# Kernel optimization log

Measured on AMD Instinct MI355X. Metric: run time of the kernel, lower is better.

## Reference

```python
import jax, jax.numpy as jnp
import numpy as np

N_HEAD = 12
N_EMBD = 768
N_EMBD_SIDE = 384
N_EMBD_KQ = 192
N_EMBD_OUT = N_EMBD + N_EMBD_SIDE  # 1152
B, L = 2, 2048


def setup_inputs() -> dict:
    key = jax.random.key(0)
    ks = jax.random.split(key, 12)
    s = 0.02
    return {
        "x": jax.random.normal(ks[0], (B, L, N_EMBD), dtype=jnp.float32),
        "side": jax.random.normal(ks[1], (B, L, N_EMBD_SIDE), dtype=jnp.float32),
        # weights stored as (in_features, out_features) so y = x @ W + b
        "Wq": jax.random.normal(ks[2], (N_EMBD_SIDE, N_EMBD_KQ), dtype=jnp.float32) * s,
        "bq": jnp.zeros((N_EMBD_KQ,), dtype=jnp.float32),
        "Wkv": jax.random.normal(ks[3], (N_EMBD_OUT, N_EMBD_KQ + N_EMBD_OUT), dtype=jnp.float32) * s,
        "bkv": jnp.zeros((N_EMBD_KQ + N_EMBD_OUT,), dtype=jnp.float32),
        "Wproj": jax.random.normal(ks[4], (N_EMBD_OUT, N_EMBD_OUT), dtype=jnp.float32) * s,
        "bproj": jnp.zeros((N_EMBD_OUT,), dtype=jnp.float32),
        "Wemb": jax.random.normal(ks[5], (N_EMBD_SIDE, N_EMBD_OUT), dtype=jnp.float32) * s,
        "bemb": jnp.zeros((N_EMBD_OUT,), dtype=jnp.float32),
    }


def reference(x, side, Wq, bq, Wkv, bkv, Wproj, bproj, Wemb, bemb):
    batch, length, _ = x.shape
    hd_kq = N_EMBD_KQ // N_HEAD   # 16
    hd_v = N_EMBD_OUT // N_HEAD   # 96

    q = (side @ Wq + bq).reshape(batch, length, N_HEAD, hd_kq).transpose(0, 2, 1, 3)  # [B,H,L,dk]
    kv = jnp.concatenate((x, side), axis=2) @ Wkv + bkv
    k = kv[:, :, :N_EMBD_KQ].reshape(batch, length, N_HEAD, hd_kq).transpose(0, 2, 1, 3)
    v = kv[:, :, N_EMBD_KQ:].reshape(batch, length, N_HEAD, hd_v).transpose(0, 2, 1, 3)

    first = (side[:, 0] @ Wemb + bemb).reshape(batch, N_HEAD, 1, hd_v)  # [B,H,1,dv]

    # shifted causal mask: row i attends to j < i; row 0 copies row 1 (attends to j==0)
    mask = jnp.tril(jnp.ones((length, length), dtype=bool), k=-1)
    mask = mask.at[0].set(mask[1])

    scale = 1.0 / jnp.sqrt(jnp.asarray(hd_kq, dtype=q.dtype))
    scores = jnp.einsum("bhqd,bhkd->bhqk", q, k) * scale
    scores = jnp.where(mask, scores, -jnp.inf)
    attn = jax.nn.softmax(scores, axis=-1)
    y = jnp.einsum("bhqk,bhkd->bhqd", attn, v)  # [B,H,L,dv]

    # special-case first token: replaced by learned embedding of side[:,0]
    y = jnp.concatenate((first, y[:, :, 1:]), axis=2)
    y = y.transpose(0, 2, 1, 3).reshape(batch, length, N_EMBD_OUT)
    return y @ Wproj + bproj
```

## Files before the change

### kernel.cpp

```cpp
#include <hip/hip_runtime.h>
#include <hip/hip_bf16.h>
#include <math.h>

#define N_HEADS 12
#define L_SEQ   2048
#define BATCH   2
#define D_KQ    192
#define D_OUT   1152
#define D_KV    1344
#define D_X     768
#define D_SIDE  384
#define HD_K    16
#define HD_V    96
#define M_ROWS  4096

typedef __attribute__((ext_vector_type(8))) short bf16x8;
typedef __attribute__((ext_vector_type(4))) float f32x4;

__device__ inline float  b2f(ushort u){ union{uint i; float f;} v; v.i=(uint)u<<16; return v.f; }
__device__ inline ushort f2b(float f){ __hip_bfloat16 h = __float2bfloat16(f);
                                       return *reinterpret_cast<ushort*>(&h); }

__device__ inline void gload_lds16(const ushort* g, ushort* l) {
    __builtin_amdgcn_global_load_lds(
        (const __attribute__((address_space(1))) void*)g,
        (__attribute__((address_space(3))) void*)l, 16, 0, 0);
}

#define SWZ(r, c) ((((r) * 64) + (c)) ^ (((r) & 7) << 3))

__global__ __launch_bounds__(256)
void cvt_f32_bf16(const float* __restrict__ src, int sstride,
                  ushort* __restrict__ dst, int dstride, int w4, int rows) {
    int gid = blockIdx.x * 256 + threadIdx.x;
    if (gid >= w4 * rows) return;
    int r = gid / w4, c = gid - r * w4;
    float4 v = *reinterpret_cast<const float4*>(&src[(size_t)r * sstride + c * 4]);
    ushort4 o = make_ushort4(f2b(v.x), f2b(v.y), f2b(v.z), f2b(v.w));
    *reinterpret_cast<ushort4*>(&dst[(size_t)r * dstride + c * 4]) = o;
}

__global__ __launch_bounds__(256)
void transpose_cvt(const float* __restrict__ W, ushort* __restrict__ Wt,
                   int K, int N, int Npad) {
    __shared__ float t[32][33];
    const int n0 = blockIdx.x * 32, k0 = blockIdx.y * 32;
    const int tx = threadIdx.x & 31, ty = threadIdx.x >> 5;
#pragma unroll
    for (int i = 0; i < 4; i++) {
        int n = n0 + tx;
        t[ty + i * 8][tx] = (n < N) ? W[(size_t)(k0 + ty + i * 8) * N + n] : 0.f;
    }
    __syncthreads();
#pragma unroll
    for (int i = 0; i < 4; i++) {
        int n = n0 + ty + i * 8;
        Wt[(size_t)n * K + k0 + tx] = f2b(t[tx][ty + i * 8]);
    }
}

template<int STORE_BF16>
__global__ __launch_bounds__(256)
void gemm_mfma(const ushort* __restrict__ A, const ushort* __restrict__ Bt,
               const float* __restrict__ bias, void* __restrict__ Cv,
               int M, int N, int K) {
    __shared__ ushort As[128 * 32];
    __shared__ ushort Bs[128 * 32];
    const int tid = threadIdx.x;
    const int w = tid >> 6, lane = tid & 63;
    const int wr = w >> 1, wc = w & 1;
    const int n0 = blockIdx.x * 128, m0 = blockIdx.y * 128;
    const int l4 = lane & 3, lrow = lane >> 2;
    const int kgrp = lane >> 4, l16 = lane & 15;

    f32x4 acc[4][4];
#pragma unroll
    for (int i = 0; i < 4; i++)
#pragma unroll
        for (int j = 0; j < 4; j++)
            acc[i][j] = (f32x4){0.f, 0.f, 0.f, 0.f};

    for (int kt = 0; kt < K; kt += 32) {
        __syncthreads();
#pragma unroll
        for (int r = 0; r < 2; r++) {
            const int seg = r * 4 + w;
            const int trow = seg * 16 + lrow;
            gload_lds16(&A [(size_t)(m0 + trow) * K + kt + l4 * 8], &As[seg * 512]);
            gload_lds16(&Bt[(size_t)(n0 + trow) * K + kt + l4 * 8], &Bs[seg * 512]);
        }
        __syncthreads();

        bf16x8 a[4], b[4];
#pragma unroll
        for (int i = 0; i < 4; i++)
            a[i] = *reinterpret_cast<const bf16x8*>(
                &As[(wr * 64 + i * 16 + l16) * 32 + kgrp * 8]);
#pragma unroll
        for (int j = 0; j < 4; j++)
            b[j] = *reinterpret_cast<const bf16x8*>(
                &Bs[(wc * 64 + j * 16 + l16) * 32 + kgrp * 8]);
#pragma unroll
        for (int i = 0; i < 4; i++)
#pragma unroll
            for (int j = 0; j < 4; j++)
                acc[i][j] = __builtin_amdgcn_mfma_f32_16x16x32_bf16(
                    a[i], b[j], acc[i][j], 0, 0, 0);
    }

    const int rgrp = lane >> 4;
#pragma unroll
    for (int j = 0; j < 4; j++) {
        const int col = n0 + wc * 64 + j * 16 + l16;
        if (col >= N) continue;
        const float bv = bias[col];
#pragma unroll
        for (int i = 0; i < 4; i++) {
            const int row0 = m0 + wr * 64 + i * 16 + rgrp * 4;
#pragma unroll
            for (int rg = 0; rg < 4; rg++) {
                float v = acc[i][j][rg] + bv;
                if (STORE_BF16)
                    ((ushort*)Cv)[(size_t)(row0 + rg) * N + col] = f2b(v);
                else
                    ((float*)Cv)[(size_t)(row0 + rg) * N + col] = v;
            }
        }
    }
}

__global__ __launch_bounds__(256)
void attn_mfma(const ushort* __restrict__ qb, const ushort* __restrict__ kvb,
               ushort* __restrict__ yb) {
    __shared__ ushort Ks2[64 * 40];
    __shared__ ushort Vt[96 * 64];
    __shared__ ushort Ps[4][16 * 64];

    const int tid  = threadIdx.x;
    const int w    = tid >> 6, lane = tid & 63;
    const int l16  = lane & 15, kgrp = lane >> 4;

    const int item = blockIdx.x;
    const int qt = item & 31, hb = item >> 5;
    const int h  = hb % N_HEADS, b = hb / N_HEADS;

    const ushort* kvbase = kvb + (size_t)b * L_SEQ * D_KV;
    const int rowbase = qt * 64;

    bf16x8 qf = {0, 0, 0, 0, 0, 0, 0, 0};
    if (kgrp < 2)
        qf = *reinterpret_cast<const bf16x8*>(
            qb + ((size_t)b * L_SEQ + rowbase + w * 16 + l16) * D_KQ + h * HD_K + kgrp * 8);

    float m[4] = {-INFINITY, -INFINITY, -INFINITY, -INFINITY};
    float l[4] = {0.f, 0.f, 0.f, 0.f};
    f32x4 acc[6];
#pragma unroll
    for (int ob = 0; ob < 6; ob++) acc[ob] = (f32x4){0.f, 0.f, 0.f, 0.f};

    for (int t2 = 0; t2 <= qt; t2++) {
        const int j0 = t2 * 64;
        const bool diag = (t2 == qt);
        __syncthreads();

        {
            const int key = tid >> 2, c = (tid & 3) * 4;
            ushort4 k4 = *reinterpret_cast<const ushort4*>(
                kvbase + (size_t)(j0 + key) * D_KV + h * HD_K + c);
            *reinterpret_cast<ushort4*>(&Ks2[key * 40 + c])      = k4;
            *reinterpret_cast<ushort4*>(&Ks2[key * 40 + 16 + c]) = make_ushort4(0, 0, 0, 0);
        }
        {
            const int key = tid >> 2, d0 = (tid & 3) * 24;
            const uint4* vsrc = reinterpret_cast<const uint4*>(
                kvbase + (size_t)(j0 + key) * D_KV + D_KQ + h * HD_V + d0);
#pragma unroll
            for (int ch = 0; ch < 3; ch++) {
                uint4 u = vsrc[ch];
                const int d = d0 + ch * 8;
                Vt[SWZ(d + 0, key)] = (ushort)(u.x & 0xffff);
                Vt[SWZ(d + 1, key)] = (ushort)(u.x >> 16);
                Vt[SWZ(d + 2, key)] = (ushort)(u.y & 0xffff);
                Vt[SWZ(d + 3, key)] = (ushort)(u.y >> 16);
                Vt[SWZ(d + 4, key)] = (ushort)(u.z & 0xffff);
                Vt[SWZ(d + 5, key)] = (ushort)(u.z >> 16);
                Vt[SWZ(d + 6, key)] = (ushort)(u.w & 0xffff);
                Vt[SWZ(d + 7, key)] = (ushort)(u.w >> 16);
            }
        }
        __syncthreads();

        f32x4 s[4];
#pragma unroll
        for (int f = 0; f < 4; f++) {
            bf16x8 kf = *reinterpret_cast<const bf16x8*>(
                &Ks2[(f * 16 + l16) * 40 + kgrp * 8]);
            s[f] = __builtin_amdgcn_mfma_f32_16x16x32_bf16(
                qf, kf, (f32x4){0.f, 0.f, 0.f, 0.f}, 0, 0, 0);
        }

#pragma unroll
        for (int f = 0; f < 4; f++)
#pragma unroll
            for (int r = 0; r < 4; r++) {
                float v = s[f][r] * 0.25f;
                if (diag) {
                    const int row64 = w * 16 + kgrp * 4 + r;
                    const int key64 = f * 16 + l16;
                    if (key64 >= row64) v = -INFINITY;
                }
                s[f][r] = v;
            }

        float scl[4];
#pragma unroll
        for (int r = 0; r < 4; r++) {
            float mt = fmaxf(fmaxf(s[0][r], s[1][r]), fmaxf(s[2][r], s[3][r]));
            mt = fmaxf(mt, __shfl_xor(mt, 1));
            mt = fmaxf(mt, __shfl_xor(mt, 2));
            mt = fmaxf(mt, __shfl_xor(mt, 4));
            mt = fmaxf(mt, __shfl_xor(mt, 8));
            const float mn = fmaxf(m[r], mt);
            scl[r] = __expf(m[r] - mn);
            m[r] = mn;
            float ps = 0.f;
#pragma unroll
            for (int f = 0; f < 4; f++) {
                float p = __expf(s[f][r] - mn);
                s[f][r] = p;
                ps += p;
            }
            ps += __shfl_xor(ps, 1);
            ps += __shfl_xor(ps, 2);
            ps += __shfl_xor(ps, 4);
            ps += __shfl_xor(ps, 8);
            l[r] = l[r] * scl[r] + ps;
        }

#pragma unroll
        for (int f = 0; f < 4; f++)
#pragma unroll
            for (int r = 0; r < 4; r++)
                Ps[w][SWZ(kgrp * 4 + r, f * 16 + l16)] = f2b(s[f][r]);
#pragma unroll
        for (int ob = 0; ob < 6; ob++)
#pragma unroll
            for (int r = 0; r < 4; r++)
                acc[ob][r] *= scl[r];

        asm volatile("s_waitcnt lgkmcnt(0)" ::: "memory");
        __builtin_amdgcn_sched_barrier(0);

        bf16x8 pa0 = *reinterpret_cast<const bf16x8*>(&Ps[w][SWZ(l16, kgrp * 8)]);
        bf16x8 pa1 = *reinterpret_cast<const bf16x8*>(&Ps[w][SWZ(l16, 32 + kgrp * 8)]);
#pragma unroll
        for (int ob = 0; ob < 6; ob++) {
            bf16x8 vb0 = *reinterpret_cast<const bf16x8*>(&Vt[SWZ(ob * 16 + l16, kgrp * 8)]);
            bf16x8 vb1 = *reinterpret_cast<const bf16x8*>(&Vt[SWZ(ob * 16 + l16, 32 + kgrp * 8)]);
            acc[ob] = __builtin_amdgcn_mfma_f32_16x16x32_bf16(pa0, vb0, acc[ob], 0, 0, 0);
            acc[ob] = __builtin_amdgcn_mfma_f32_16x16x32_bf16(pa1, vb1, acc[ob], 0, 0, 0);
        }
    }

#pragma unroll
    for (int r = 0; r < 4; r++) {
        const float inv = 1.f / l[r];
        ushort* dst = yb + ((size_t)b * L_SEQ + rowbase + w * 16 + kgrp * 4 + r) * D_OUT
                        + h * HD_V;
#pragma unroll
        for (int ob = 0; ob < 6; ob++)
            dst[ob * 16 + l16] = f2b(acc[ob][r] * inv);
    }
}

__global__ __launch_bounds__(128)
void first_kernel(const float* __restrict__ side, const float* __restrict__ Wemb,
                  const float* __restrict__ bemb, ushort* __restrict__ yb) {
    const int o = blockIdx.x * 128 + threadIdx.x;
    const int b = blockIdx.y;
    const float* s = side + (size_t)b * L_SEQ * D_SIDE;
    float acc = bemb[o];
    for (int k = 0; k < D_SIDE; k++)
        acc += s[k] * Wemb[(size_t)k * D_OUT + o];
    yb[(size_t)b * L_SEQ * D_OUT + o] = f2b(acc);
}

extern "C" void kernel_launch(void* const* d_in, const int* in_sizes, int n_in,
                              void* d_out, int out_size, void* d_ws, size_t ws_size,
                              hipStream_t stream) {
    const float* x     = (const float*)d_in[0];
    const float* side  = (const float*)d_in[1];
    const float* Wq    = (const float*)d_in[2];
    const float* bq    = (const float*)d_in[3];
    const float* Wkv   = (const float*)d_in[4];
    const float* bkv   = (const float*)d_in[5];
    const float* Wproj = (const float*)d_in[6];
    const float* bproj = (const float*)d_in[7];
    const float* Wemb  = (const float*)d_in[8];
    const float* bemb  = (const float*)d_in[9];
    float* out = (float*)d_out;

    char* ws = (char*)d_ws;
    ushort* xs_bf   = (ushort*)(ws + 0);
    ushort* side_bf = (ushort*)(ws + 9437184);
    ushort* wq_t    = (ushort*)(ws + 12582912);
    ushort* wkv_t   = (ushort*)(ws + 12779520);
    ushort* wproj_t = (ushort*)(ws + 16023552);
    ushort* qbuf    = (ushort*)(ws + 18677760);
    ushort* kvbuf   = (ushort*)(ws + 20250624);
    ushort* ybuf    = (ushort*)(ws + 31260672);

    {
        int items_x  = (D_X / 4) * M_ROWS;
        int items_sd = (D_SIDE / 4) * M_ROWS;
        cvt_f32_bf16<<<(items_x  + 255) / 256, 256, 0, stream>>>(
            x,    D_X,    xs_bf,       D_OUT,  D_X / 4,    M_ROWS);
        cvt_f32_bf16<<<(items_sd + 255) / 256, 256, 0, stream>>>(
            side, D_SIDE, xs_bf + D_X, D_OUT,  D_SIDE / 4, M_ROWS);
        cvt_f32_bf16<<<(items_sd + 255) / 256, 256, 0, stream>>>(
            side, D_SIDE, side_bf,     D_SIDE, D_SIDE / 4, M_ROWS);
    }
    transpose_cvt<<<dim3(8, 12),  256, 0, stream>>>(Wq,    wq_t,    D_SIDE, D_KQ,  256);
    transpose_cvt<<<dim3(44, 36), 256, 0, stream>>>(Wkv,   wkv_t,   D_OUT,  D_KV,  1408);
    transpose_cvt<<<dim3(36, 36), 256, 0, stream>>>(Wproj, wproj_t, D_OUT,  D_OUT, 1152);

    gemm_mfma<1><<<dim3(2, 32),  256, 0, stream>>>(side_bf, wq_t,    bq,    qbuf,  M_ROWS, D_KQ,  D_SIDE);
    gemm_mfma<1><<<dim3(11, 32), 256, 0, stream>>>(xs_bf,   wkv_t,   bkv,   kvbuf, M_ROWS, D_KV,  D_OUT);
    attn_mfma<<<768, 256, 0, stream>>>(qbuf, kvbuf, ybuf);
    first_kernel<<<dim3(9, BATCH), 128, 0, stream>>>(side, Wemb, bemb, ybuf);
    gemm_mfma<0><<<dim3(9, 32),  256, 0, stream>>>(ybuf,    wproj_t, bproj, out,   M_ROWS, D_OUT, D_OUT);
}
```

Before: 321.9 us.

## Emit transposed V and separate K from KV GEMM; DMA tiles into LDS

The KV projection GEMM now writes K to its own row-major buffer and V pre-transposed per (batch, head) into a swizzled-compatible layout. The attention kernel can then fill its K and V tiles with direct global-to-LDS loads instead of scalar transposing stores. The attention grid is also remapped so heavy and light causal tiles are interleaved, and MFMA sections are bracketed with s_setprio. The risk is less coalesced epilogue stores in the GEMM, which writes V with strided ushort4 stores, and correctness depends on the voff swizzle matching SWZ.

Measured after the change: 280.1 us. -13.0%, faster.

```diff
diff --git a/kernel.cpp b/kernel.cpp
--- a/kernel.cpp
+++ b/kernel.cpp
@@ -59,11 +59,11 @@
     }
 }
 
-template<int STORE_BF16>
+template<int MODE>
 __global__ __launch_bounds__(256)
 void gemm_mfma(const ushort* __restrict__ A, const ushort* __restrict__ Bt,
                const float* __restrict__ bias, void* __restrict__ Cv,
-               int M, int N, int K) {
+               ushort* __restrict__ vt, int M, int N, int K) {
     __shared__ ushort As[128 * 32];
     __shared__ ushort Bs[128 * 32];
     const int tid = threadIdx.x;
@@ -114,13 +114,40 @@
         const int col = n0 + wc * 64 + j * 16 + l16;
         if (col >= N) continue;
         const float bv = bias[col];
+        if constexpr (MODE == 2) {
+            if (col >= D_KQ) {
+                const int hh = (col - D_KQ) / HD_V;
+                const int dd = (col - D_KQ) % HD_V;
+                const int bb = m0 >> 11;
+                ushort* vrow = vt + ((size_t)(bb * N_HEADS + hh) * HD_V + dd) * L_SEQ
+                                  + (m0 & 2047);
+#pragma unroll
+                for (int i = 0; i < 4; i++) {
+                    const int r0 = wr * 64 + i * 16 + rgrp * 4;
+                    ushort4 o = make_ushort4(
+                        f2b(acc[i][j][0] + bv), f2b(acc[i][j][1] + bv),
+                        f2b(acc[i][j][2] + bv), f2b(acc[i][j][3] + bv));
+                    *reinterpret_cast<ushort4*>(&vrow[r0]) = o;
+                }
+                continue;
+            }
+#pragma unroll
+            for (int i = 0; i < 4; i++) {
+                const int row0 = m0 + wr * 64 + i * 16 + rgrp * 4;
+#pragma unroll
+                for (int rg = 0; rg < 4; rg++)
+                    ((ushort*)Cv)[(size_t)(row0 + rg) * D_KQ + col] =
+                        f2b(acc[i][j][rg] + bv);
+            }
+            continue;
+        }
 #pragma unroll
         for (int i = 0; i < 4; i++) {
             const int row0 = m0 + wr * 64 + i * 16 + rgrp * 4;
 #pragma unroll
             for (int rg = 0; rg < 4; rg++) {
                 float v = acc[i][j][rg] + bv;
-                if (STORE_BF16)
+                if (MODE == 1)
                     ((ushort*)Cv)[(size_t)(row0 + rg) * N + col] = f2b(v);
                 else
                     ((float*)Cv)[(size_t)(row0 + rg) * N + col] = v;
@@ -130,27 +157,47 @@
 }
 
 __global__ __launch_bounds__(256)
-void attn_mfma(const ushort* __restrict__ qb, const ushort* __restrict__ kvb,
-               ushort* __restrict__ yb) {
-    __shared__ ushort Ks2[64 * 40];
+void attn_mfma(const ushort* __restrict__ qbuf, const ushort* __restrict__ kb,
+               const ushort* __restrict__ vtg, ushort* __restrict__ yb) {
     __shared__ ushort Vt[96 * 64];
+    __shared__ ushort Ks[64 * 16];
+    __shared__ __align__(16) ushort Kz[8];
     __shared__ ushort Ps[4][16 * 64];
 
-    const int tid  = threadIdx.x;
-    const int w    = tid >> 6, lane = tid & 63;
-    const int l16  = lane & 15, kgrp = lane >> 4;
-
-    const int item = blockIdx.x;
-    const int qt = item & 31, hb = item >> 5;
-    const int h  = hb % N_HEADS, b = hb / N_HEADS;
-
-    const ushort* kvbase = kvb + (size_t)b * L_SEQ * D_KV;
+    const int tid = threadIdx.x;
+    const int w = tid >> 6, lane = tid & 63;
+    const int l16 = lane & 15, kgrp = lane >> 4;
+
+    const int i = blockIdx.x, jj5 = i & 255, g = i >> 8;
+    const int q5 = jj5 & 31;
+    const int qt = (g == 0) ? q5 : (g == 1) ? (31 - q5) : ((q5 + 16) & 31);
+    const int hb = g * 8 + (jj5 >> 5);
+    const int h = hb % N_HEADS, b = hb / N_HEADS;
+
+    if (tid < 8) Kz[tid] = 0;
+
+    const ushort* vt_h  = vtg + (size_t)(b * N_HEADS + h) * HD_V * L_SEQ;
+    const ushort* kbase = kb + (size_t)b * L_SEQ * D_KQ;
     const int rowbase = qt * 64;
+
+    int voff[3];
+#pragma unroll
+    for (int s3 = 0; s3 < 3; s3++) {
+        const int L = (w * 3 + s3) * 1024 + lane * 16;
+        const int X = L ^ (((L >> 7) & 7) << 4);
+        voff[s3] = (X >> 7) * L_SEQ + ((X >> 1) & 63);
+    }
+    int koff = 0;
+    if (w < 2) {
+        const int elem = (w * 1024 + lane * 16) >> 1;
+        koff = (elem >> 4) * D_KQ + h * HD_K + ((elem >> 3) & 1) * 8;
+    }
 
     bf16x8 qf = {0, 0, 0, 0, 0, 0, 0, 0};
     if (kgrp < 2)
         qf = *reinterpret_cast<const bf16x8*>(
-            qb + ((size_t)b * L_SEQ + rowbase + w * 16 + l16) * D_KQ + h * HD_K + kgrp * 8);
+            qbuf + ((size_t)b * L_SEQ + rowbase + w * 16 + l16) * D_KQ
+                 + h * HD_K + kgrp * 8);
 
     float m[4] = {-INFINITY, -INFINITY, -INFINITY, -INFINITY};
     float l[4] = {0.f, 0.f, 0.f, 0.f};
@@ -163,41 +210,24 @@
         const bool diag = (t2 == qt);
         __syncthreads();
 
-        {
-            const int key = tid >> 2, c = (tid & 3) * 4;
-            ushort4 k4 = *reinterpret_cast<const ushort4*>(
-                kvbase + (size_t)(j0 + key) * D_KV + h * HD_K + c);
-            *reinterpret_cast<ushort4*>(&Ks2[key * 40 + c])      = k4;
-            *reinterpret_cast<ushort4*>(&Ks2[key * 40 + 16 + c]) = make_ushort4(0, 0, 0, 0);
-        }
-        {
-            const int key = tid >> 2, d0 = (tid & 3) * 24;
-            const uint4* vsrc = reinterpret_cast<const uint4*>(
-                kvbase + (size_t)(j0 + key) * D_KV + D_KQ + h * HD_V + d0);
-#pragma unroll
-            for (int ch = 0; ch < 3; ch++) {
-                uint4 u = vsrc[ch];
-                const int d = d0 + ch * 8;
-                Vt[SWZ(d + 0, key)] = (ushort)(u.x & 0xffff);
-                Vt[SWZ(d + 1, key)] = (ushort)(u.x >> 16);
-                Vt[SWZ(d + 2, key)] = (ushort)(u.y & 0xffff);
-                Vt[SWZ(d + 3, key)] = (ushort)(u.y >> 16);
-                Vt[SWZ(d + 4, key)] = (ushort)(u.z & 0xffff);
-                Vt[SWZ(d + 5, key)] = (ushort)(u.z >> 16);
-                Vt[SWZ(d + 6, key)] = (ushort)(u.w & 0xffff);
-                Vt[SWZ(d + 7, key)] = (ushort)(u.w >> 16);
-            }
-        }
+        if (w < 2)
+            gload_lds16(kbase + (size_t)j0 * D_KQ + koff, &Ks[w * 512]);
+#pragma unroll
+        for (int s3 = 0; s3 < 3; s3++)
+            gload_lds16(vt_h + voff[s3] + j0, &Vt[(w * 3 + s3) * 512]);
         __syncthreads();
 
+        __builtin_amdgcn_s_setprio(1);
         f32x4 s[4];
 #pragma unroll
         for (int f = 0; f < 4; f++) {
-            bf16x8 kf = *reinterpret_cast<const bf16x8*>(
-                &Ks2[(f * 16 + l16) * 40 + kgrp * 8]);
+            const ushort* kp = (kgrp < 2) ? &Ks[(f * 16 + l16) * 16 + kgrp * 8]
+                                          : &Kz[0];
+            bf16x8 kf = *reinterpret_cast<const bf16x8*>(kp);
             s[f] = __builtin_amdgcn_mfma_f32_16x16x32_bf16(
                 qf, kf, (f32x4){0.f, 0.f, 0.f, 0.f}, 0, 0, 0);
         }
+        __builtin_amdgcn_s_setprio(0);
 
 #pragma unroll
         for (int f = 0; f < 4; f++)
@@ -253,6 +283,7 @@
 
         bf16x8 pa0 = *reinterpret_cast<const bf16x8*>(&Ps[w][SWZ(l16, kgrp * 8)]);
         bf16x8 pa1 = *reinterpret_cast<const bf16x8*>(&Ps[w][SWZ(l16, 32 + kgrp * 8)]);
+        __builtin_amdgcn_s_setprio(1);
 #pragma unroll
         for (int ob = 0; ob < 6; ob++) {
             bf16x8 vb0 = *reinterpret_cast<const bf16x8*>(&Vt[SWZ(ob * 16 + l16, kgrp * 8)]);
@@ -260,6 +291,7 @@
             acc[ob] = __builtin_amdgcn_mfma_f32_16x16x32_bf16(pa0, vb0, acc[ob], 0, 0, 0);
             acc[ob] = __builtin_amdgcn_mfma_f32_16x16x32_bf16(pa1, vb1, acc[ob], 0, 0, 0);
         }
+        __builtin_amdgcn_s_setprio(0);
     }
 
 #pragma unroll
@@ -307,7 +339,8 @@
     ushort* wkv_t   = (ushort*)(ws + 12779520);
     ushort* wproj_t = (ushort*)(ws + 16023552);
     ushort* qbuf    = (ushort*)(ws + 18677760);
-    ushort* kvbuf   = (ushort*)(ws + 20250624);
+    ushort* kbuf    = (ushort*)(ws + 20250624);
+    ushort* vtg     = (ushort*)(ws + 21823488);
     ushort* ybuf    = (ushort*)(ws + 31260672);
 
     {
@@ -324,9 +357,12 @@
     transpose_cvt<<<dim3(44, 36), 256, 0, stream>>>(Wkv,   wkv_t,   D_OUT,  D_KV,  1408);
     transpose_cvt<<<dim3(36, 36), 256, 0, stream>>>(Wproj, wproj_t, D_OUT,  D_OUT, 1152);
 
-    gemm_mfma<1><<<dim3(2, 32),  256, 0, stream>>>(side_bf, wq_t,    bq,    qbuf,  M_ROWS, D_KQ,  D_SIDE);
-    gemm_mfma<1><<<dim3(11, 32), 256, 0, stream>>>(xs_bf,   wkv_t,   bkv,   kvbuf, M_ROWS, D_KV,  D_OUT);
-    attn_mfma<<<768, 256, 0, stream>>>(qbuf, kvbuf, ybuf);
+    gemm_mfma<1><<<dim3(2, 32),  256, 0, stream>>>(
+        side_bf, wq_t, bq, qbuf, nullptr, M_ROWS, D_KQ, D_SIDE);
+    gemm_mfma<2><<<dim3(11, 32), 256, 0, stream>>>(
+        xs_bf, wkv_t, bkv, kbuf, vtg, M_ROWS, D_KV, D_OUT);
+    attn_mfma<<<768, 256, 0, stream>>>(qbuf, kbuf, vtg, ybuf);
     first_kernel<<<dim3(9, BATCH), 128, 0, stream>>>(side, Wemb, bemb, ybuf);
-    gemm_mfma<0><<<dim3(9, 32),  256, 0, stream>>>(ybuf,    wproj_t, bproj, out,   M_ROWS, D_OUT, D_OUT);
-}
+    gemm_mfma<0><<<dim3(9, 32),  256, 0, stream>>>(
+        ybuf, wproj_t, bproj, out, nullptr, M_ROWS, D_OUT, D_OUT);
+}
```
